# Kernel tuning notes

Measured on AMD Instinct MI355X. Metric: run time of the kernel, lower is better.

The kernel has to match this reference:

```python
import jax, jax.numpy as jnp
import numpy as np

N, E = 20000, 320000
H1, C1 = 8, 128   # gat1 heads/out
H2, C2 = 1, 128   # gat2 heads/out
D_IN = 768
NEG_SLOPE = 0.2
BN_EPS = 1e-5


def setup_inputs() -> dict:
    key = jax.random.key(0)
    ks = jax.random.split(key, 16)
    def rn(k, shape, fan):
        return jax.random.normal(k, shape, dtype=jnp.float32) / np.sqrt(fan)
    x = jax.random.normal(ks[0], (N, D_IN), dtype=jnp.float32)
    edge_index = jax.random.randint(ks[1], (2, E), 0, N, dtype=jnp.int64)
    return {
        "x": x,
        "edge_index": edge_index,
        "W1": rn(ks[2], (D_IN, H1 * C1), D_IN),
        "att_src1": rn(ks[3], (H1, C1), C1),
        "att_dst1": rn(ks[4], (H1, C1), C1),
        "b1": jnp.zeros((H1 * C1,), jnp.float32),
        "W2": rn(ks[5], (H1 * C1, H2 * C2), H1 * C1),
        "att_src2": rn(ks[6], (H2, C2), C2),
        "att_dst2": rn(ks[7], (H2, C2), C2),
        "b2": jnp.zeros((C2,), jnp.float32),
        "g1": jnp.ones((H1 * C1,), jnp.float32),
        "be1": jnp.zeros((H1 * C1,), jnp.float32),
        "g2": jnp.ones((C2,), jnp.float32),
        "be2": jnp.zeros((C2,), jnp.float32),
        "Wc1": rn(ks[8], (C2, 64), C2),
        "bc1": jnp.zeros((64,), jnp.float32),
        "Wc2": rn(ks[9], (64, 2), 64),
        "bc2": jnp.zeros((2,), jnp.float32),
    }


def gat_conv(x, src, dst, W, att_src, att_dst, bias, heads, ch, concat):
    n = x.shape[0]
    h = (x @ W).reshape(n, heads, ch)                      # [N,H,C]
    a_s = jnp.sum(h * att_src[None], axis=-1)              # [N,H]
    a_d = jnp.sum(h * att_dst[None], axis=-1)
    e = a_s[src] + a_d[dst]                                # [Et,H]
    e = jax.nn.leaky_relu(e, NEG_SLOPE)
    # segment softmax over incoming edges of each dst node
    m = jax.ops.segment_max(e, dst, num_segments=n)
    ex = jnp.exp(e - m[dst])
    z = jax.ops.segment_sum(ex, dst, num_segments=n)
    alpha = ex / z[dst]                                    # [Et,H]
    msg = alpha[:, :, None] * h[src]                       # [Et,H,C]
    out = jax.ops.segment_sum(msg, dst, num_segments=n)    # [N,H,C]
    if concat:
        out = out.reshape(n, heads * ch)
    else:
        out = out.mean(axis=1)
    return out + bias


def batch_norm(x, gamma, beta):
    mu = x.mean(axis=0)
    var = x.var(axis=0)
    return (x - mu) * jax.lax.rsqrt(var + BN_EPS) * gamma + beta


def reference(x, edge_index, W1, att_src1, att_dst1, b1, W2, att_src2, att_dst2, b2,
              g1, be1, g2, be2, Wc1, bc1, Wc2, bc2):
    n = x.shape[0]
    loop = jnp.arange(n, dtype=edge_index.dtype)
    src = jnp.concatenate([edge_index[0], loop])  # PyG add_self_loops default
    dst = jnp.concatenate([edge_index[1], loop])
    h = gat_conv(x, src, dst, W1, att_src1, att_dst1, b1, H1, C1, True)
    h = jax.nn.elu(batch_norm(h, g1, be1))
    h = gat_conv(h, src, dst, W2, att_src2, att_dst2, b2, H2, C2, False)
    h = jax.nn.elu(batch_norm(h, g2, be2))
    h = jax.nn.relu(h @ Wc1 + bc1)
    return h @ Wc2 + bc2
```

## Files before the change

kernel.cpp:

```cpp
#include <hip/hip_runtime.h>
#include <hip/hip_bf16.h>
#include <math.h>

#define N_NODES 20000
#define N_EDGES 320000
#define DIN 768
#define F1 1024
#define H1 8
#define C1 128
#define F2 128
#define NEG_SLOPE 0.2f
#define BN_EPS 1e-5f
#define RESCALE_THR 8.0f

typedef __attribute__((ext_vector_type(8))) __bf16 bf16x8;
typedef __attribute__((ext_vector_type(4))) float f32x4;

__device__ __forceinline__ float leaky(float x) { return x > 0.f ? x : NEG_SLOPE * x; }

__device__ __forceinline__ unsigned short f2bu(float x) {
  __hip_bfloat16 b = __float2bfloat16(x);
  return *(unsigned short*)&b;
}
__device__ __forceinline__ float b2f(unsigned short u) {
  return __uint_as_float(((unsigned)u) << 16);
}
__device__ __forceinline__ unsigned pack2(float lo, float hi) {
  return (unsigned)f2bu(lo) | ((unsigned)f2bu(hi) << 16);
}

__device__ __forceinline__ void async_copy16(void* lds, const void* g) {
  __builtin_amdgcn_global_load_lds(
      (const __attribute__((address_space(1))) unsigned int*)g,
      (__attribute__((address_space(3))) unsigned int*)lds, 16, 0, 0);
}

__global__ void repack_hist_kernel(const int* raw, int* ei32, int* deg) {
  int is64 = (raw[1] == 0 && raw[3] == 0 && raw[5] == 0 && raw[7] == 0) ? 1 : 0;
  int e = blockIdx.x * blockDim.x + threadIdx.x;
  if (e < 2 * N_EDGES) {
    int v = is64 ? raw[2 * e] : raw[e];
    ei32[e] = v;
    if (e >= N_EDGES) atomicAdd(&deg[v], 1);
  }
}

#define NPT 20
__global__ __launch_bounds__(1024) void scan_kernel(const int* __restrict__ deg,
                                                    int* __restrict__ off,
                                                    int* __restrict__ cursor) {
  __shared__ int wsum[16];
  int tid = threadIdx.x;
  int lane = tid & 63, wv = tid >> 6;
  int base = tid * NPT;
  int loc[NPT];
  int run = 0;
#pragma unroll
  for (int k = 0; k < NPT; ++k) {
    int i = base + k;
    int v = (i < N_NODES) ? deg[i] : 0;
    loc[k] = run;
    run += v;
  }
  int incl = run;
  for (int sh = 1; sh < 64; sh <<= 1) {
    int t = __shfl_up(incl, sh, 64);
    if (lane >= sh) incl += t;
  }
  if (lane == 63) wsum[wv] = incl;
  __syncthreads();
  if (wv == 0 && lane < 16) {
    int v = wsum[lane];
    for (int sh = 1; sh < 16; sh <<= 1) {
      int t = __shfl_up(v, sh, 16);
      if (lane >= sh) v += t;
    }
    wsum[lane] = v;
  }
  __syncthreads();
  int wbase = (wv > 0) ? wsum[wv - 1] : 0;
  int tbase = wbase + incl - run;
#pragma unroll
  for (int k = 0; k < NPT; ++k) {
    int i = base + k;
    if (i < N_NODES) {
      int o = tbase + loc[k];
      off[i] = o;
      cursor[i] = o;
    }
  }
  if (tid == 1023) off[N_NODES] = wbase + incl;
}

__global__ void scatter_kernel(const int* ei, int* cursor, int* elist) {
  int e = blockIdx.x * blockDim.x + threadIdx.x;
  if (e < N_EDGES) {
    int dst = ei[N_EDGES + e];
    int p = atomicAdd(&cursor[dst], 1);
    elist[p] = ei[e];
  }
}

__global__ void f2b_kernel(const float* __restrict__ in, unsigned short* __restrict__ out,
                           size_t n4) {
  size_t i = (size_t)blockIdx.x * blockDim.x + threadIdx.x;
  size_t stride = (size_t)gridDim.x * blockDim.x;
  for (; i < n4; i += stride) {
    float4 v = ((const float4*)in)[i];
    ushort4 u;
    u.x = f2bu(v.x); u.y = f2bu(v.y); u.z = f2bu(v.z); u.w = f2bu(v.w);
    ((ushort4*)out)[i] = u;
  }
}

__global__ void transpose_b_kernel(const float* __restrict__ W, unsigned short* __restrict__ WT,
                                   int K, int N) {
  __shared__ float t[32][33];
  int k0 = blockIdx.y * 32, n0 = blockIdx.x * 32;
  int tx = threadIdx.x & 31, ty = threadIdx.x >> 5;
  for (int i = 0; i < 32; i += 8)
    t[ty + i][tx] = W[(size_t)(k0 + ty + i) * N + n0 + tx];
  __syncthreads();
  for (int i = 0; i < 32; i += 8)
    WT[(size_t)(n0 + ty + i) * K + k0 + tx] = f2bu(t[tx][ty + i]);
}

#define GBM 128
#define GBN 128
#define GBK 64
template <int H, int SWZ>
__global__ __launch_bounds__(256) void mfma_gemm_att_kernel(
    const unsigned short* __restrict__ A,
    const unsigned short* __restrict__ BT,
    unsigned short* __restrict__ C,
    const float* __restrict__ att_src,
    const float* __restrict__ att_dst,
    float* __restrict__ as_out,
    float* __restrict__ ad_out,
    int M, int N, int K) {
  __shared__ __hip_bfloat16 As[GBM][GBK];
  __shared__ __hip_bfloat16 Bs[GBN][GBK];
  __shared__ float sred[128][2];
  __shared__ float dred[128][2];
  int bx, by;
  if (SWZ) {
    int bid = blockIdx.x;
    int pl = bid & 7, c = (bid >> 3) & 7, ph = bid >> 6;
    int p = ph * 8 + pl;
    if (p * GBM >= M) return;
    by = p; bx = c;
  } else {
    bx = blockIdx.x; by = blockIdx.y;
  }
  int tid = threadIdx.x;
  int lane = tid & 63, wid = tid >> 6;
  int wr = wid >> 1, wc = wid & 1;
  int row0 = by * GBM, col0 = bx * GBN;
  int head = bx;
  int l16 = lane & 15, l4 = lane >> 4;
  f32x4 acc[4][4] = {};
  for (int k0 = 0; k0 < K; k0 += GBK) {
#pragma unroll
    for (int j = 0; j < 4; ++j) {
      int c = j * 256 + tid;
      int r = c >> 3, kk = (c & 7) << 3;
      int ga = row0 + r; if (ga >= M) ga = M - 1;
      async_copy16(&As[r][kk], A + (size_t)ga * K + k0 + kk);
      async_copy16(&Bs[r][kk], BT + (size_t)(col0 + r) * K + k0 + kk);
    }
    __syncthreads();
#pragma unroll
    for (int ks = 0; ks < 2; ++ks) {
      bf16x8 af[4], bfr[4];
#pragma unroll
      for (int i = 0; i < 4; ++i)
        af[i] = *(const bf16x8*)&As[wr * 64 + i * 16 + l16][ks * 32 + l4 * 8];
#pragma unroll
      for (int j = 0; j < 4; ++j)
        bfr[j] = *(const bf16x8*)&Bs[wc * 64 + j * 16 + l16][ks * 32 + l4 * 8];
#pragma unroll
      for (int i = 0; i < 4; ++i)
#pragma unroll
        for (int j = 0; j < 4; ++j)
          acc[i][j] = __builtin_amdgcn_mfma_f32_16x16x32_bf16(af[i], bfr[j], acc[i][j], 0, 0, 0);
    }
    __syncthreads();
  }
#pragma unroll
  for (int i = 0; i < 4; ++i) {
#pragma unroll
    for (int j = 0; j < 4; ++j) {
#pragma unroll
      for (int r = 0; r < 4; ++r) {
        int row = row0 + wr * 64 + i * 16 + l4 * 4 + r;
        int col = col0 + wc * 64 + j * 16 + l16;
        if (row < M) C[(size_t)row * N + col] = f2bu(acc[i][j][r]);
      }
    }
  }
  float avs[4], avd[4];
#pragma unroll
  for (int j = 0; j < 4; ++j) {
    int col = col0 + wc * 64 + j * 16 + l16;
    avs[j] = att_src[col];
    avd[j] = att_dst[col];
  }
#pragma unroll
  for (int i = 0; i < 4; ++i) {
#pragma unroll
    for (int r = 0; r < 4; ++r) {
      float ps = 0.f, pd = 0.f;
#pragma unroll
      for (int j = 0; j < 4; ++j) { ps += acc[i][j][r] * avs[j]; pd += acc[i][j][r] * avd[j]; }
#pragma unroll
      for (int mk = 1; mk < 16; mk <<= 1) {
        ps += __shfl_xor(ps, mk, 64);
        pd += __shfl_xor(pd, mk, 64);
      }
      if (l16 == 0) {
        int lr = wr * 64 + i * 16 + l4 * 4 + r;
        sred[lr][wc] = ps;
        dred[lr][wc] = pd;
      }
    }
  }
  __syncthreads();
  if (tid < 128) {
    int row = row0 + tid;
    if (row < M) {
      as_out[(size_t)row * H + head] = sred[tid][0] + sred[tid][1];
      ad_out[(size_t)row * H + head] = dred[tid][0] + dred[tid][1];
    }
  }
}

#define G1_LOAD(i, rv, ev)                                                     \
  if ((i) < e) {                                                               \
    int ssrc = elist[(i)];                                                     \
    ev = leaky(as1[ssrc * H1 + head] + ad);                                    \
    rv = *(const unsigned*)(h1 + (size_t)ssrc * F1 + cb);                      \
  }
#define G1_CONSUME(u, el)                                                      \
  {                                                                            \
    float w;                                                                   \
    if (el > m + RESCALE_THR) {                                                \
      float rr = __expf(m - el);                                               \
      z *= rr; a0 *= rr; a1 *= rr;                                             \
      m = el; w = 1.f;                                                         \
    } else {                                                                   \
      w = __expf(el - m);                                                      \
    }                                                                          \
    z += w;                                                                    \
    a0 += w * __uint_as_float(u << 16);                                        \
    a1 += w * __uint_as_float(u & 0xffff0000u);                                \
  }

__global__ __launch_bounds__(64) void gather1_kernel(const unsigned short* __restrict__ h1,
                                                     const float* __restrict__ as1,
                                                     const float* __restrict__ ad1,
                                                     const int* __restrict__ off,
                                                     const int* __restrict__ elist,
                                                     const float* __restrict__ b1,
                                                     unsigned short* __restrict__ out1) {
  int head = blockIdx.x;
  int node = blockIdx.y;
  int tid = threadIdx.x;
  int cb = head * C1 + tid * 2;
  const float ad = ad1[node * H1 + head];
  int s = off[node], e = off[node + 1];
  float m = leaky(as1[node * H1 + head] + ad);
  float z = 1.f;
  float a0, a1;
  {
    unsigned u = *(const unsigned*)(h1 + (size_t)node * F1 + cb);
    a0 = __uint_as_float(u << 16); a1 = __uint_as_float(u & 0xffff0000u);
  }
  unsigned ra0 = 0, ra1 = 0, ra2 = 0, ra3 = 0;
  float ea0 = 0.f, ea1 = 0.f, ea2 = 0.f, ea3 = 0.f;
  G1_LOAD(s + 0, ra0, ea0)
  G1_LOAD(s + 1, ra1, ea1)
  G1_LOAD(s + 2, ra2, ea2)
  G1_LOAD(s + 3, ra3, ea3)
  for (int base = s; base < e; base += 4) {
    unsigned rb0 = 0, rb1 = 0, rb2 = 0, rb3 = 0;
    float eb0 = 0.f, eb1 = 0.f, eb2 = 0.f, eb3 = 0.f;
    int nb = base + 4;
    G1_LOAD(nb + 0, rb0, eb0)
    G1_LOAD(nb + 1, rb1, eb1)
    G1_LOAD(nb + 2, rb2, eb2)
    G1_LOAD(nb + 3, rb3, eb3)
    G1_CONSUME(ra0, ea0)
    if (base + 1 < e) G1_CONSUME(ra1, ea1)
    if (base + 2 < e) G1_CONSUME(ra2, ea2)
    if (base + 3 < e) G1_CONSUME(ra3, ea3)
    ra0 = rb0; ra1 = rb1; ra2 = rb2; ra3 = rb3;
    ea0 = eb0; ea1 = eb1; ea2 = eb2; ea3 = eb3;
  }
  float inv = 1.f / z;
  float2 bv = *(const float2*)(b1 + cb);
  unsigned o = pack2(a0 * inv + bv.x, a1 * inv + bv.y);
  *(unsigned*)(out1 + (size_t)node * F1 + cb) = o;
}

__global__ void bnstats_bf16_kernel(const unsigned short* __restrict__ x,
                                    float* __restrict__ sums,
                                    int nrows, int F, int rowsPerBlock) {
  int tid = threadIdx.x;
  int c = tid * 4;
  int r0 = blockIdx.x * rowsPerBlock;
  int rend = min(r0 + rowsPerBlock, nrows);
  float s0 = 0.f, s1 = 0.f, s2 = 0.f, s3 = 0.f;
  float q0 = 0.f, q1 = 0.f, q2 = 0.f, q3 = 0.f;
  for (int r = r0; r < rend; ++r) {
    ushort4 u = *(const ushort4*)(x + (size_t)r * F + c);
    float v0 = b2f(u.x), v1 = b2f(u.y), v2 = b2f(u.z), v3 = b2f(u.w);
    s0 += v0; s1 += v1; s2 += v2; s3 += v3;
    q0 += v0 * v0; q1 += v1 * v1; q2 += v2 * v2; q3 += v3 * v3;
  }
  atomicAdd(&sums[c + 0], s0); atomicAdd(&sums[c + 1], s1);
  atomicAdd(&sums[c + 2], s2); atomicAdd(&sums[c + 3], s3);
  atomicAdd(&sums[F + c + 0], q0); atomicAdd(&sums[F + c + 1], q1);
  atomicAdd(&sums[F + c + 2], q2); atomicAdd(&sums[F + c + 3], q3);
}

template <int CPT>
__global__ void bnstats_kernel(const float* __restrict__ x, float* __restrict__ sums,
                               int nrows, int F, int rowsPerBlock) {
  int tid = threadIdx.x;
  int r0 = blockIdx.x * rowsPerBlock;
  int rend = min(r0 + rowsPerBlock, nrows);
  float s[CPT], q[CPT];
#pragma unroll
  for (int k = 0; k < CPT; ++k) { s[k] = 0.f; q[k] = 0.f; }
  for (int r = r0; r < rend; ++r) {
    const float* row = x + (size_t)r * F;
#pragma unroll
    for (int k = 0; k < CPT; ++k) {
      float v = row[tid + k * blockDim.x];
      s[k] += v; q[k] += v * v;
    }
  }
#pragma unroll
  for (int k = 0; k < CPT; ++k) {
    atomicAdd(&sums[tid + k * blockDim.x], s[k]);
    atomicAdd(&sums[F + tid + k * blockDim.x], q[k]);
  }
}

__global__ void bnfinal_kernel(const float* __restrict__ sums, const float* __restrict__ g,
                               const float* __restrict__ be, float* __restrict__ ss, int F) {
  int c = blockIdx.x * blockDim.x + threadIdx.x;
  if (c < F) {
    float mu = sums[c] * (1.f / N_NODES);
    float var = sums[F + c] * (1.f / N_NODES) - mu * mu;
    float sc = g[c] * rsqrtf(var + BN_EPS);
    ss[c] = sc;
    ss[F + c] = be[c] - mu * sc;
  }
}

__global__ void bnapply_bf16_kernel(unsigned short* __restrict__ x, const float* __restrict__ ss,
                                    int F, size_t total4) {
  size_t i = (size_t)blockIdx.x * blockDim.x + threadIdx.x;
  size_t stride = (size_t)gridDim.x * blockDim.x;
  for (; i < total4; i += stride) {
    int c = (int)((i * 4) & (size_t)(F - 1));
    ushort4 u = ((ushort4*)x)[i];
    float v0 = b2f(u.x) * ss[c + 0] + ss[F + c + 0];
    float v1 = b2f(u.y) * ss[c + 1] + ss[F + c + 1];
    float v2 = b2f(u.z) * ss[c + 2] + ss[F + c + 2];
    float v3 = b2f(u.w) * ss[c + 3] + ss[F + c + 3];
    v0 = v0 > 0.f ? v0 : expm1f(v0);
    v1 = v1 > 0.f ? v1 : expm1f(v1);
    v2 = v2 > 0.f ? v2 : expm1f(v2);
    v3 = v3 > 0.f ? v3 : expm1f(v3);
    u.x = f2bu(v0); u.y = f2bu(v1); u.z = f2bu(v2); u.w = f2bu(v3);
    ((ushort4*)x)[i] = u;
  }
}

#define G2_LOAD(i, rv, ev)                                                     \
  if ((i) < e) {                                                               \
    int ssrc = elist[(i)];                                                     \
    ev = leaky(as2[ssrc] + ad);                                                \
    rv = *(const unsigned*)(h2 + (size_t)ssrc * F2 + tid * 2);                 \
  }
#define G2_CONSUME(u, el)                                                      \
  {                                                                            \
    float w;                                                                   \
    if (el > m + RESCALE_THR) {                                                \
      float rr = __expf(m - el);                                               \
      z *= rr; a0 *= rr; a1 *= rr;                                             \
      m = el; w = 1.f;                                                         \
    } else {                                                                   \
      w = __expf(el - m);                                                      \
    }                                                                          \
    z += w;                                                                    \
    a0 += w * __uint_as_float(u << 16);                                        \
    a1 += w * __uint_as_float(u & 0xffff0000u);                                \
  }

__global__ __launch_bounds__(64) void gather2_kernel(const unsigned short* __restrict__ h2,
                                                     const float* __restrict__ as2,
                                                     const float* __restrict__ ad2,
                                                     const int* __restrict__ off,
                                                     const int* __restrict__ elist,
                                                     const float* __restrict__ b2,
                                                     float* __restrict__ out2) {
  int node = blockIdx.x;
  int tid = threadIdx.x;
  const float ad = ad2[node];
  int s = off[node], e = off[node + 1];
  float m = leaky(as2[node] + ad);
  float z = 1.f;
  float a0, a1;
  {
    unsigned u = *(const unsigned*)(h2 + (size_t)node * F2 + tid * 2);
    a0 = __uint_as_float(u << 16); a1 = __uint_as_float(u & 0xffff0000u);
  }
  unsigned ra0 = 0, ra1 = 0, ra2 = 0, ra3 = 0;
  float ea0 = 0.f, ea1 = 0.f, ea2 = 0.f, ea3 = 0.f;
  G2_LOAD(s + 0, ra0, ea0)
  G2_LOAD(s + 1, ra1, ea1)
  G2_LOAD(s + 2, ra2, ea2)
  G2_LOAD(s + 3, ra3, ea3)
  for (int base = s; base < e; base += 4) {
    unsigned rb0 = 0, rb1 = 0, rb2 = 0, rb3 = 0;
    float eb0 = 0.f, eb1 = 0.f, eb2 = 0.f, eb3 = 0.f;
    int nb = base + 4;
    G2_LOAD(nb + 0, rb0, eb0)
    G2_LOAD(nb + 1, rb1, eb1)
    G2_LOAD(nb + 2, rb2, eb2)
    G2_LOAD(nb + 3, rb3, eb3)
    G2_CONSUME(ra0, ea0)
    if (base + 1 < e) G2_CONSUME(ra1, ea1)
    if (base + 2 < e) G2_CONSUME(ra2, ea2)
    if (base + 3 < e) G2_CONSUME(ra3, ea3)
    ra0 = rb0; ra1 = rb1; ra2 = rb2; ra3 = rb3;
    ea0 = eb0; ea1 = eb1; ea2 = eb2; ea3 = eb3;
  }
  float inv = 1.f / z;
  float2 o = make_float2(a0 * inv + b2[tid * 2 + 0], a1 * inv + b2[tid * 2 + 1]);
  *(float2*)(out2 + (size_t)node * F2 + tid * 2) = o;
}

__global__ __launch_bounds__(64) void cls_kernel(const float* __restrict__ h,
                                                 const float* __restrict__ ss2,
                                                 const float* __restrict__ Wc1,
                                                 const float* __restrict__ bc1,
                                                 const float* __restrict__ Wc2,
                                                 const float* __restrict__ bc2,
                                                 float* __restrict__ out) {
  __shared__ float hl[128];
  int node = blockIdx.x;
  int tid = threadIdx.x;
  {
    float v = h[(size_t)node * F2 + tid] * ss2[tid] + ss2[F2 + tid];
    v = v > 0.f ? v : expm1f(v);
    hl[tid] = v;
    float v2 = h[(size_t)node * F2 + 64 + tid] * ss2[64 + tid] + ss2[F2 + 64 + tid];
    v2 = v2 > 0.f ? v2 : expm1f(v2);
    hl[tid + 64] = v2;
  }
  __syncthreads();
  float acc = bc1[tid];
#pragma unroll
  for (int k = 0; k < 128; ++k) acc += hl[k] * Wc1[k * 64 + tid];
  acc = fmaxf(acc, 0.f);
  float2 w = *(const float2*)(Wc2 + tid * 2);
  float o0 = acc * w.x, o1 = acc * w.y;
  for (int sh = 32; sh >= 1; sh >>= 1) {
    o0 += __shfl_down(o0, sh, 64);
    o1 += __shfl_down(o1, sh, 64);
  }
  if (tid == 0) {
    out[node * 2 + 0] = o0 + bc2[0];
    out[node * 2 + 1] = o1 + bc2[1];
  }
}

extern "C" void kernel_launch(void* const* d_in, const int* in_sizes, int n_in,
                              void* d_out, int out_size, void* d_ws, size_t ws_size,
                              hipStream_t stream) {
  const float* x        = (const float*)d_in[0];
  const int*   ei_raw   = (const int*)d_in[1];
  const float* W1       = (const float*)d_in[2];
  const float* att_src1 = (const float*)d_in[3];
  const float* att_dst1 = (const float*)d_in[4];
  const float* b1       = (const float*)d_in[5];
  const float* W2       = (const float*)d_in[6];
  const float* att_src2 = (const float*)d_in[7];
  const float* att_dst2 = (const float*)d_in[8];
  const float* b2       = (const float*)d_in[9];
  const float* g1       = (const float*)d_in[10];
  const float* be1      = (const float*)d_in[11];
  const float* g2       = (const float*)d_in[12];
  const float* be2      = (const float*)d_in[13];
  const float* Wc1      = (const float*)d_in[14];
  const float* bc1      = (const float*)d_in[15];
  const float* Wc2      = (const float*)d_in[16];
  const float* bc2      = (const float*)d_in[17];
  float* out = (float*)d_out;

  char* ws = (char*)d_ws;
  size_t o = 0;
  unsigned short* h1b   = (unsigned short*)(ws + o); o += (size_t)N_NODES * F1 * 2;
  unsigned short* out1b = (unsigned short*)(ws + o); o += (size_t)N_NODES * F1 * 2;
  unsigned short* xb    = (unsigned short*)(ws + o); o += (size_t)N_NODES * DIN * 2;
  unsigned short* h2b   = (unsigned short*)(ws + o); o += (size_t)N_NODES * F2 * 2;
  float* out2  = (float*)(ws + o); o += (size_t)N_NODES * F2 * 4;
  float* as1   = (float*)(ws + o); o += (size_t)N_NODES * H1 * 4;
  float* ad1   = (float*)(ws + o); o += (size_t)N_NODES * H1 * 4;
  float* as2   = (float*)(ws + o); o += (size_t)N_NODES * 4;
  float* ad2   = (float*)(ws + o); o += (size_t)N_NODES * 4;
  char*  zbase = ws + o;
  float* bnsum1 = (float*)(ws + o); o += F1 * 2 * 4;
  float* bnsum2 = (float*)(ws + o); o += F2 * 2 * 4;
  int*   deg    = (int*)(ws + o); o += (size_t)N_NODES * 4;
  size_t zbytes = (size_t)((ws + o) - zbase);
  int*   offv   = (int*)(ws + o); o += (size_t)(N_NODES + 4) * 4;
  int*   cursor = (int*)(ws + o); o += (size_t)N_NODES * 4;
  int*   elist  = (int*)(ws + o); o += (size_t)N_EDGES * 4;
  float* ss1    = (float*)(ws + o); o += F1 * 2 * 4;
  float* ss2    = (float*)(ws + o); o += F2 * 2 * 4;
  int*   ei32   = (int*)(ws + o); o += (size_t)2 * N_EDGES * 4;
  unsigned short* W1T = (unsigned short*)(ws + o); o += (size_t)F1 * DIN * 2;
  unsigned short* W2T = (unsigned short*)(ws + o); o += (size_t)F2 * F1 * 2;
  (void)ws_size; (void)in_sizes; (void)n_in; (void)out_size;

  hipMemsetAsync((void*)zbase, 0, zbytes, stream);

  f2b_kernel<<<2048, 256, 0, stream>>>(x, xb, (size_t)N_NODES * DIN / 4);
  {
    dim3 g1d(F1 / 32, DIN / 32);
    transpose_b_kernel<<<g1d, 256, 0, stream>>>(W1, W1T, DIN, F1);
    dim3 g2d(F2 / 32, F1 / 32);
    transpose_b_kernel<<<g2d, 256, 0, stream>>>(W2, W2T, F1, F2);
  }

  repack_hist_kernel<<<(2 * N_EDGES + 255) / 256, 256, 0, stream>>>(ei_raw, ei32, deg);
  scan_kernel<<<1, 1024, 0, stream>>>(deg, offv, cursor);
  scatter_kernel<<<(N_EDGES + 255) / 256, 256, 0, stream>>>(ei32, cursor, elist);

  {
    int panels = (N_NODES + GBM - 1) / GBM;
    int grid1 = ((panels + 7) / 8) * 64;
    mfma_gemm_att_kernel<H1, 1><<<grid1, 256, 0, stream>>>(
        xb, W1T, h1b, att_src1, att_dst1, as1, ad1, N_NODES, F1, DIN);
  }
  gather1_kernel<<<dim3(H1, N_NODES), 64, 0, stream>>>(h1b, as1, ad1, offv, elist, b1, out1b);
  {
    int rows = 79;
    int grid = (N_NODES + rows - 1) / rows;
    bnstats_bf16_kernel<<<grid, 256, 0, stream>>>(out1b, bnsum1, N_NODES, F1, rows);
  }
  bnfinal_kernel<<<(F1 + 255) / 256, 256, 0, stream>>>(bnsum1, g1, be1, ss1, F1);
  bnapply_bf16_kernel<<<2048, 256, 0, stream>>>(out1b, ss1, F1, (size_t)N_NODES * F1 / 4);

  {
    dim3 grid(F2 / GBN, (N_NODES + GBM - 1) / GBM);
    mfma_gemm_att_kernel<1, 0><<<grid, 256, 0, stream>>>(
        out1b, W2T, h2b, att_src2, att_dst2, as2, ad2, N_NODES, F2, F1);
  }
  gather2_kernel<<<N_NODES, 64, 0, stream>>>(h2b, as2, ad2, offv, elist, b2, out2);
  {
    int rows = 79;
    int grid = (N_NODES + rows - 1) / rows;
    bnstats_kernel<1><<<grid, 128, 0, stream>>>(out2, bnsum2, N_NODES, F2, rows);
  }
  bnfinal_kernel<<<1, F2, 0, stream>>>(bnsum2, g2, be2, ss2, F2);

  cls_kernel<<<N_NODES, 64, 0, stream>>>(out2, ss2, Wc1, bc1, Wc2, bc2, out);
}
```

Baseline: 477.1 us.

## Precompute layer-1 softmax weights in separate kernel before feature gather

Splits the layer-1 GAT aggregation into two passes. A new per-node kernel computes the exact segment max, the exponentiated edge weights (stored head-major), the normalizer inverse and the self-loop weight. The gather kernel then only does weighted accumulation with no online-softmax rescaling branches. This removes the redundant per-channel exp and branch work, at the cost of an extra launch and a 10 MB write and read of edge weights.

```diff
diff --git a/kernel.cpp b/kernel.cpp
--- a/kernel.cpp
+++ b/kernel.cpp
@@ -234,69 +234,96 @@
   }
 }
 
-#define G1_LOAD(i, rv, ev)                                                     \
+__global__ __launch_bounds__(64) void alpha1_kernel(const float* __restrict__ as1,
+                                                    const float* __restrict__ ad1,
+                                                    const int* __restrict__ off,
+                                                    const int* __restrict__ elist,
+                                                    float* __restrict__ wexpT,
+                                                    float* __restrict__ zinv,
+                                                    float* __restrict__ wself) {
+  int node = blockIdx.x;
+  int lane = threadIdx.x;
+  int s = off[node], e = off[node + 1];
+#pragma unroll
+  for (int h = 0; h < H1; ++h) {
+    float ad = ad1[node * H1 + h];
+    float selfl = leaky(as1[node * H1 + h] + ad);
+    float m = selfl;
+    for (int i = s + lane; i < e; i += 64) {
+      float el = leaky(as1[elist[i] * H1 + h] + ad);
+      m = fmaxf(m, el);
+    }
+    for (int sh = 32; sh >= 1; sh >>= 1) m = fmaxf(m, __shfl_xor(m, sh, 64));
+    float z = 0.f;
+    for (int i = s + lane; i < e; i += 64) {
+      float el = leaky(as1[elist[i] * H1 + h] + ad);
+      float w = __expf(el - m);
+      wexpT[(size_t)h * N_EDGES + i] = w;
+      z += w;
+    }
+    for (int sh = 32; sh >= 1; sh >>= 1) z += __shfl_xor(z, sh, 64);
+    float ws = __expf(selfl - m);
+    if (lane == 0) {
+      zinv[node * H1 + h] = 1.f / (z + ws);
+      wself[node * H1 + h] = ws;
+    }
+  }
+}
+
+#define GW_LOAD(i, rv, wv)                                                     \
   if ((i) < e) {                                                               \
-    int ssrc = elist[(i)];                                                     \
-    ev = leaky(as1[ssrc * H1 + head] + ad);                                    \
-    rv = *(const unsigned*)(h1 + (size_t)ssrc * F1 + cb);                      \
-  }
-#define G1_CONSUME(u, el)                                                      \
+    wv = wp[(i)];                                                              \
+    rv = *(const unsigned*)(h1 + (size_t)elist[(i)] * F1 + cb);                \
+  }
+#define GW_CONS(u, wv)                                                         \
   {                                                                            \
-    float w;                                                                   \
-    if (el > m + RESCALE_THR) {                                                \
-      float rr = __expf(m - el);                                               \
-      z *= rr; a0 *= rr; a1 *= rr;                                             \
-      m = el; w = 1.f;                                                         \
-    } else {                                                                   \
-      w = __expf(el - m);                                                      \
-    }                                                                          \
-    z += w;                                                                    \
-    a0 += w * __uint_as_float(u << 16);                                        \
-    a1 += w * __uint_as_float(u & 0xffff0000u);                                \
-  }
-
-__global__ __launch_bounds__(64) void gather1_kernel(const unsigned short* __restrict__ h1,
-                                                     const float* __restrict__ as1,
-                                                     const float* __restrict__ ad1,
-                                                     const int* __restrict__ off,
-                                                     const int* __restrict__ elist,
-                                                     const float* __restrict__ b1,
-                                                     unsigned short* __restrict__ out1) {
+    a0 += wv * __uint_as_float(u << 16);                                       \
+    a1 += wv * __uint_as_float(u & 0xffff0000u);                               \
+  }
+
+__global__ __launch_bounds__(64) void gatherw1_kernel(const unsigned short* __restrict__ h1,
+                                                      const float* __restrict__ wexpT,
+                                                      const float* __restrict__ zinv,
+                                                      const float* __restrict__ wself,
+                                                      const int* __restrict__ off,
+                                                      const int* __restrict__ elist,
+                                                      const float* __restrict__ b1,
+                                                      unsigned short* __restrict__ out1) {
   int head = blockIdx.x;
   int node = blockIdx.y;
   int tid = threadIdx.x;
   int cb = head * C1 + tid * 2;
-  const float ad = ad1[node * H1 + head];
   int s = off[node], e = off[node + 1];
-  float m = leaky(as1[node * H1 + head] + ad);
-  float z = 1.f;
+  const float* wp = wexpT + (size_t)head * N_EDGES;
   float a0, a1;
   {
+    float ws = wself[node * H1 + head];
     unsigned u = *(const unsigned*)(h1 + (size_t)node * F1 + cb);
-    a0 = __uint_as_float(u << 16); a1 = __uint_as_float(u & 0xffff0000u);
+    a0 = ws * __uint_as_float(u << 16);
+    a1 = ws * __uint_as_float(u & 0xffff0000u);
   }
   unsigned ra0 = 0, ra1 = 0, ra2 = 0, ra3 = 0;
-  float ea0 = 0.f, ea1 = 0.f, ea2 = 0.f, ea3 = 0.f;
-  G1_LOAD(s + 0, ra0, ea0)
-  G1_LOAD(s + 1, ra1, ea1)
-  G1_LOAD(s + 2, ra2, ea2)
-  G1_LOAD(s + 3, ra3, ea3)
+  float wa0 = 0.f, wa1 = 0.f, wa2 = 0.f, wa3 = 0.f;
+  GW_LOAD(s + 0, ra0, wa0)
+  GW_LOAD(s + 1, ra1, wa1)
+  GW_LOAD(s + 2, ra2, wa2)
+  GW_LOAD(s + 3, ra3, wa3)
   for (int base = s; base < e; base += 4) {
     unsigned rb0 = 0, rb1 = 0, rb2 = 0, rb3 = 0;
-    float eb0 = 0.f, eb1 = 0.f, eb2 = 0.f, eb3 = 0.f;
+    float wb0 = 0.f, wb1 = 0.f, wb2 = 0.f, wb3 = 0.f;
     int nb = base + 4;
-    G1_LOAD(nb + 0, rb0, eb0)
-    G1_LOAD(nb + 1, rb1, eb1)
-    G1_LOAD(nb + 2, rb2, eb2)
-    G1_LOAD(nb + 3, rb3, eb3)
-    G1_CONSUME(ra0, ea0)
-    if (base + 1 < e) G1_CONSUME(ra1, ea1)
-    if (base + 2 < e) G1_CONSUME(ra2, ea2)
-    if (base + 3 < e) G1_CONSUME(ra3, ea3)
+    GW_LOAD(nb + 0, rb0, wb0)
+    GW_LOAD(nb + 1, rb1, wb1)
+    GW_LOAD(nb + 2, rb2, wb2)
+    GW_LOAD(nb + 3, rb3, wb3)
+    GW_CONS(ra0, wa0)
+    GW_CONS(ra1, wa1)
+    GW_CONS(ra2, wa2)
+    GW_CONS(ra3, wa3)
     ra0 = rb0; ra1 = rb1; ra2 = rb2; ra3 = rb3;
-    ea0 = eb0; ea1 = eb1; ea2 = eb2; ea3 = eb3;
-  }
-  float inv = 1.f / z;
+    wa0 = wb0; wa1 = wb1; wa2 = wb2; wa3 = wb3;
+  }
+  float inv = zinv[node * H1 + head];
   float2 bv = *(const float2*)(b1 + cb);
   unsigned o = pack2(a0 * inv + bv.x, a1 * inv + bv.y);
   *(unsigned*)(out1 + (size_t)node * F1 + cb) = o;
@@ -513,6 +540,9 @@
   float* ad1   = (float*)(ws + o); o += (size_t)N_NODES * H1 * 4;
   float* as2   = (float*)(ws + o); o += (size_t)N_NODES * 4;
   float* ad2   = (float*)(ws + o); o += (size_t)N_NODES * 4;
+  float* wexpT = (float*)(ws + o); o += (size_t)H1 * N_EDGES * 4;
+  float* zinv  = (float*)(ws + o); o += (size_t)N_NODES * H1 * 4;
+  float* wself = (float*)(ws + o); o += (size_t)N_NODES * H1 * 4;
   char*  zbase = ws + o;
   float* bnsum1 = (float*)(ws + o); o += F1 * 2 * 4;
   float* bnsum2 = (float*)(ws + o); o += F2 * 2 * 4;
@@ -548,7 +578,9 @@
     mfma_gemm_att_kernel<H1, 1><<<grid1, 256, 0, stream>>>(
         xb, W1T, h1b, att_src1, att_dst1, as1, ad1, N_NODES, F1, DIN);
   }
-  gather1_kernel<<<dim3(H1, N_NODES), 64, 0, stream>>>(h1b, as1, ad1, offv, elist, b1, out1b);
+  alpha1_kernel<<<N_NODES, 64, 0, stream>>>(as1, ad1, offv, elist, wexpT, zinv, wself);
+  gatherw1_kernel<<<dim3(H1, N_NODES), 64, 0, stream>>>(
+      h1b, wexpT, zinv, wself, offv, elist, b1, out1b);
   {
     int rows = 79;
     int grid = (N_NODES + rows - 1) / rows;
```

Result: faster. 461.7 us (-3.2%).
